# Optimization experiments

Hardware: AMD Instinct MI355X
Metric: run time of the kernel (lower is better)

## Reference

```python
import jax, jax.numpy as jnp
import numpy as np
import heapq

VOCAB = 50257
EMBED = 128
SEED = 0


def _build_padded_paths(vocab_size: int, seed: int):
    """Build a Huffman tree over random word counts and return padded
    per-leaf path index / code / mask arrays: [V, max_depth]."""
    rng = np.random.default_rng(seed)
    counts = rng.integers(1, 1000, size=vocab_size).astype(np.int64)
    # node = (value, left, right); leaves: 0..V-1, internal: V..2V-2
    heap = [(int(counts[i]), i, (i, None, None)) for i in range(vocab_size)]
    heapq.heapify(heap)
    nv = vocab_size
    while len(heap) > 1:
        c1, _, n1 = heapq.heappop(heap)
        c2, _, n2 = heapq.heappop(heap)
        heapq.heappush(heap, (c1 + c2, nv, (nv, n1, n2)))
        nv += 1
    root = heap[0][2]
    assert root[0] == 2 * vocab_size - 2
    path_idx = [None] * vocab_size
    path_code = [None] * vocab_size
    stack = [(root, [], [])]
    while stack:
        (val, left, right), idx, code = stack.pop()
        if left is None:  # leaf
            path_idx[val] = idx
            path_code[val] = code
        else:
            ni = idx + [val - vocab_size]
            stack.append((left, ni, code + [0.0]))
            stack.append((right, ni, code + [1.0]))
    max_d = max(len(p) for p in path_idx)
    I = np.zeros((vocab_size, max_d), dtype=np.int32)
    C = np.zeros((vocab_size, max_d), dtype=np.float32)
    M = np.zeros((vocab_size, max_d), dtype=np.float32)
    for v in range(vocab_size):
        L = len(path_idx[v])
        I[v, :L] = path_idx[v]
        C[v, :L] = path_code[v]
        M[v, :L] = 1.0
    return jnp.asarray(I), jnp.asarray(C), jnp.asarray(M)


def setup_inputs() -> dict:
    key = jax.random.key(0)
    k1, k2, k3 = jax.random.split(key, 3)
    embedding = jax.random.normal(k1, (128, 1, 256, EMBED), dtype=jnp.float32)
    target = jax.random.randint(k2, (128, 1, 256), 0, VOCAB, dtype=jnp.int32)
    fc = jax.random.uniform(k3, (VOCAB - 1, EMBED), dtype=jnp.float32)  # torch.rand init
    path_idx, path_code, path_mask = _build_padded_paths(VOCAB, SEED)
    return {"embedding": embedding, "target": target, "fc": fc,
            "path_idx": path_idx, "path_code": path_code, "path_mask": path_mask}


def reference(embedding, target, fc, path_idx, path_code, path_mask):
    emb = embedding.reshape(-1, embedding.shape[-1])          # [T, H]
    t = target.reshape(-1)                                     # [T]
    idx = path_idx[t]                                          # [T, D]
    code = path_code[t]                                        # [T, D]
    mask = path_mask[t]                                        # [T, D]
    w = fc[idx]                                                # [T, D, H] gathered rows
    logits = jnp.einsum('th,tdh->td', emb, w)                  # [T, D]
    # binary_cross_entropy_with_logits, elementwise, stable
    bce = jnp.maximum(logits, 0.0) - logits * code + jnp.log1p(jnp.exp(-jnp.abs(logits)))
    return jnp.sum(bce * mask) / jnp.sum(mask)
```

## Files before the change

### kernel.cpp

```cpp
#include <hip/hip_runtime.h>

#define TILE    16
#define BLOCK   256
#define EMBED   128
#define VOCAB   50257
#define ESTRIDE 132
#define NPART   2048

__global__ __launch_bounds__(256) void hs_pack(
    const float* __restrict__ fc, ushort* __restrict__ out, int n)
{
    const int stride = gridDim.x * 256 * 8;
    for (int i = (blockIdx.x * 256 + threadIdx.x) * 8; i < n; i += stride) {
        const uint4 a = *(const uint4*)(fc + i);
        const uint4 b = *(const uint4*)(fc + i + 4);
        ushort r[8];
        const uint* u = &a.x;
        #pragma unroll
        for (int j = 0; j < 4; ++j)
            r[j] = (ushort)((u[j] + 0x7FFFu + ((u[j] >> 16) & 1u)) >> 16);
        const uint* v = &b.x;
        #pragma unroll
        for (int j = 0; j < 4; ++j)
            r[4 + j] = (ushort)((v[j] + 0x7FFFu + ((v[j] >> 16) & 1u)) >> 16);
        *(uint4*)(out + i) = *(uint4*)r;
    }
}

__global__ __launch_bounds__(BLOCK) void hs_main_bf16(
    const float* __restrict__ emb,
    const int*   __restrict__ target,
    const ushort* __restrict__ fcb,
    const int*   __restrict__ path_idx,
    const float* __restrict__ path_code,
    const float* __restrict__ path_mask,
    int T, int D,
    float* __restrict__ partial_b,
    float* __restrict__ partial_c)
{
    extern __shared__ char smem[];
    float* se  = (float*)smem;
    int2*  sic = (int2*)(smem + TILE * ESTRIDE * 4);
    __shared__ float sb[BLOCK / 64];
    __shared__ float sc[BLOCK / 64];

    const int tok0 = blockIdx.x * TILE;
    const int ntok = min(TILE, T - tok0);

    const float4* g4 = (const float4*)(emb + (size_t)tok0 * EMBED);
    for (int j = threadIdx.x; j < TILE * (EMBED / 4); j += BLOCK) {
        const int f = j * 4, tk = f >> 7, kk = f & 127;
        float4 v = make_float4(0.f, 0.f, 0.f, 0.f);
        if (tk < ntok) v = g4[j];
        *(float4*)&se[tk * ESTRIDE + kk] = v;
    }
    for (int j = threadIdx.x; j < TILE * D; j += BLOCK) {
        const int tk = j & (TILE - 1), d = j >> 4;
        int2 m = make_int2(0, __float_as_int(-1.0f));
        if (tk < ntok) {
            const int v = target[tok0 + tk];
            const size_t po = (size_t)v * D + d;
            if (path_mask[po] != 0.f)
                m = make_int2(path_idx[po], __float_as_int(path_code[po]));
        }
        sic[j] = m;
    }
    __syncthreads();

    const int wave = threadIdx.x >> 6;
    const int g    = (threadIdx.x >> 2) & 15;
    const int sub  = threadIdx.x & 3;

    float accb = 0.f, accc = 0.f;

    const int items = TILE * D;
    for (int it = wave * 16; it < items; it += 64) {
        const int item = it + g;
        const int2 m = sic[item];
        const float code = __int_as_float(m.y);
        if (code >= 0.f) {
            const char*   wrow = (const char*)(fcb + (size_t)m.x * EMBED);
            const float4* e4   = (const float4*)&se[g * ESTRIDE];
            float s0 = 0.f, s1 = 0.f;
            #pragma unroll
            for (int k = 0; k < 4; ++k) {
                const int c8 = k * 4 + sub;
                const uint4  wv = *(const uint4*)(wrow + (c8 << 4));
                const float4 ea = e4[c8 * 2];
                const float4 eb = e4[c8 * 2 + 1];
                s0 = fmaf(ea.x, __uint_as_float(wv.x << 16),        s0);
                s1 = fmaf(ea.y, __uint_as_float(wv.x & 0xFFFF0000u), s1);
                s0 = fmaf(ea.z, __uint_as_float(wv.y << 16),        s0);
                s1 = fmaf(ea.w, __uint_as_float(wv.y & 0xFFFF0000u), s1);
                s0 = fmaf(eb.x, __uint_as_float(wv.z << 16),        s0);
                s1 = fmaf(eb.y, __uint_as_float(wv.z & 0xFFFF0000u), s1);
                s0 = fmaf(eb.z, __uint_as_float(wv.w << 16),        s0);
                s1 = fmaf(eb.w, __uint_as_float(wv.w & 0xFFFF0000u), s1);
            }
            float x = s0 + s1;
            x += __shfl_xor(x, 1);
            x += __shfl_xor(x, 2);
            accb += fmaxf(x, 0.f) - x * code + __logf(1.f + __expf(-fabsf(x)));
            accc += 1.f;
        }
    }

    #pragma unroll
    for (int o = 32; o > 0; o >>= 1) {
        accb += __shfl_xor(accb, o);
        accc += __shfl_xor(accc, o);
    }
    const int lane = threadIdx.x & 63;
    if (lane == 0) { sb[wave] = accb; sc[wave] = accc; }
    __syncthreads();
    if (threadIdx.x == 0) {
        float b = 0.f, c = 0.f;
        #pragma unroll
        for (int i = 0; i < BLOCK / 64; ++i) { b += sb[i]; c += sc[i]; }
        partial_b[blockIdx.x] = b;
        partial_c[blockIdx.x] = c;
    }
}

__global__ __launch_bounds__(BLOCK) void hs_main_f32(
    const float* __restrict__ emb, const int* __restrict__ target,
    const float* __restrict__ fc,  const int* __restrict__ path_idx,
    const float* __restrict__ path_code, const float* __restrict__ path_mask,
    int T, int D, float* __restrict__ partial_b, float* __restrict__ partial_c)
{
    extern __shared__ char smem[];
    float* se  = (float*)smem;
    int2*  sic = (int2*)(smem + TILE * ESTRIDE * 4);
    __shared__ float sb[BLOCK / 64];
    __shared__ float sc[BLOCK / 64];

    const int tok0 = blockIdx.x * TILE;
    const int ntok = min(TILE, T - tok0);

    const float4* g4 = (const float4*)(emb + (size_t)tok0 * EMBED);
    for (int j = threadIdx.x; j < TILE * (EMBED / 4); j += BLOCK) {
        const int f = j * 4, tk = f >> 7, kk = f & 127;
        float4 v = make_float4(0.f, 0.f, 0.f, 0.f);
        if (tk < ntok) v = g4[j];
        *(float4*)&se[tk * ESTRIDE + kk] = v;
    }
    for (int j = threadIdx.x; j < TILE * D; j += BLOCK) {
        const int tk = j & (TILE - 1), d = j >> 4;
        int2 m = make_int2(0, __float_as_int(-1.0f));
        if (tk < ntok) {
            const int v = target[tok0 + tk];
            const size_t po = (size_t)v * D + d;
            if (path_mask[po] != 0.f)
                m = make_int2(path_idx[po], __float_as_int(path_code[po]));
        }
        sic[j] = m;
    }
    __syncthreads();

    const int wave = threadIdx.x >> 6;
    const int g    = (threadIdx.x >> 2) & 15;
    const int sub  = threadIdx.x & 3;
    float accb = 0.f, accc = 0.f;

    const int items = TILE * D;
    for (int it = wave * 16; it < items; it += 64) {
        const int item = it + g;
        const int2 m = sic[item];
        const float code = __int_as_float(m.y);
        if (code >= 0.f) {
            const float4* w4 = (const float4*)(fc + (size_t)m.x * EMBED);
            const float4* e4 = (const float4*)&se[g * ESTRIDE];
            float s0 = 0.f, s1 = 0.f, s2 = 0.f, s3 = 0.f;
            #pragma unroll
            for (int k = 0; k < 8; ++k) {
                const float4 w  = w4[k * 4 + sub];
                const float4 ev = e4[k * 4 + sub];
                s0 = fmaf(ev.x, w.x, s0); s1 = fmaf(ev.y, w.y, s1);
                s2 = fmaf(ev.z, w.z, s2); s3 = fmaf(ev.w, w.w, s3);
            }
            float x = (s0 + s1) + (s2 + s3);
            x += __shfl_xor(x, 1); x += __shfl_xor(x, 2);
            accb += fmaxf(x, 0.f) - x * code + __logf(1.f + __expf(-fabsf(x)));
            accc += 1.f;
        }
    }
    #pragma unroll
    for (int o = 32; o > 0; o >>= 1) {
        accb += __shfl_xor(accb, o);
        accc += __shfl_xor(accc, o);
    }
    const int lane = threadIdx.x & 63;
    if (lane == 0) { sb[wave] = accb; sc[wave] = accc; }
    __syncthreads();
    if (threadIdx.x == 0) {
        float b = 0.f, c = 0.f;
        #pragma unroll
        for (int i = 0; i < BLOCK / 64; ++i) { b += sb[i]; c += sc[i]; }
        partial_b[blockIdx.x] = b;
        partial_c[blockIdx.x] = c;
    }
}

__global__ __launch_bounds__(256) void hs_finalize(
    const float* __restrict__ pb, const float* __restrict__ pc,
    int n, float* __restrict__ out)
{
    __shared__ double rb[256];
    __shared__ double rc[256];
    double sbv = 0.0, scv = 0.0;
    for (int i = threadIdx.x; i < n; i += 256) {
        sbv += (double)pb[i];
        scv += (double)pc[i];
    }
    rb[threadIdx.x] = sbv; rc[threadIdx.x] = scv;
    __syncthreads();
    for (int s = 128; s > 0; s >>= 1) {
        if (threadIdx.x < s) {
            rb[threadIdx.x] += rb[threadIdx.x + s];
            rc[threadIdx.x] += rc[threadIdx.x + s];
        }
        __syncthreads();
    }
    if (threadIdx.x == 0) out[0] = (float)(rb[0] / rc[0]);
}

extern "C" void kernel_launch(void* const* d_in, const int* in_sizes, int n_in,
                              void* d_out, int out_size, void* d_ws, size_t ws_size,
                              hipStream_t stream) {
    const float* emb   = (const float*)d_in[0];
    const int*   tgt   = (const int*)  d_in[1];
    const float* fc    = (const float*)d_in[2];
    const int*   pidx  = (const int*)  d_in[3];
    const float* pcode = (const float*)d_in[4];
    const float* pmask = (const float*)d_in[5];

    const int T   = in_sizes[1];
    const int D   = in_sizes[3] / VOCAB;
    const int nfc = in_sizes[2];

    const int nblocks = (T + TILE - 1) / TILE;
    const size_t shmem = (size_t)TILE * ESTRIDE * 4 + (size_t)TILE * D * 8;

    float* pb = (float*)d_ws;
    float* pc = pb + NPART;
    ushort* fcb = (ushort*)((char*)d_ws + 2 * NPART * sizeof(float));
    const size_t need = 2 * NPART * sizeof(float) + (size_t)nfc * sizeof(ushort);
    float* out = (float*)d_out;

    if (ws_size >= need) {
        hs_pack<<<1024, 256, 0, stream>>>(fc, fcb, nfc);
        hs_main_bf16<<<nblocks, BLOCK, shmem, stream>>>(
            emb, tgt, fcb, pidx, pcode, pmask, T, D, pb, pc);
    } else {
        hs_main_f32<<<nblocks, BLOCK, shmem, stream>>>(
            emb, tgt, fc, pidx, pcode, pmask, T, D, pb, pc);
    }
    hs_finalize<<<1, 256, 0, stream>>>(pb, pc, nblocks, out);
}
```

Before: 35.50 us.

## Prefetch all path-row gathers up front with fully unrolled templated kernel

```diff
diff --git a/kernel.cpp b/kernel.cpp
--- a/kernel.cpp
+++ b/kernel.cpp
@@ -27,7 +27,8 @@
     }
 }
 
-__global__ __launch_bounds__(BLOCK) void hs_main_bf16(
+template <int NITER>
+__global__ __launch_bounds__(BLOCK) void hs_main_pipe(
     const float* __restrict__ emb,
     const int*   __restrict__ target,
     const ushort* __restrict__ fcb,
@@ -38,6 +39,114 @@
     float* __restrict__ partial_b,
     float* __restrict__ partial_c)
 {
+    constexpr int DP = NITER * 4;
+    extern __shared__ char smem[];
+    float* se  = (float*)smem;
+    int2*  sic = (int2*)(smem + TILE * ESTRIDE * 4);
+    __shared__ float sb[BLOCK / 64];
+    __shared__ float sc[BLOCK / 64];
+
+    const int tok0 = blockIdx.x * TILE;
+    const int ntok = min(TILE, T - tok0);
+
+    const float4* g4 = (const float4*)(emb + (size_t)tok0 * EMBED);
+    for (int j = threadIdx.x; j < TILE * (EMBED / 4); j += BLOCK) {
+        const int f = j * 4, tk = f >> 7, kk = f & 127;
+        float4 v = make_float4(0.f, 0.f, 0.f, 0.f);
+        if (tk < ntok) v = g4[j];
+        *(float4*)&se[tk * ESTRIDE + kk] = v;
+    }
+    for (int j = threadIdx.x; j < TILE * DP; j += BLOCK) {
+        const int tk = j & (TILE - 1), d = j >> 4;
+        int2 m = make_int2(0, __float_as_int(-1.0f));
+        if (tk < ntok && d < D) {
+            const int v = target[tok0 + tk];
+            const size_t po = (size_t)v * D + d;
+            if (path_mask[po] != 0.f)
+                m = make_int2(path_idx[po], __float_as_int(path_code[po]));
+        }
+        sic[j] = m;
+    }
+    __syncthreads();
+
+    const int wave = threadIdx.x >> 6;
+    const int g    = (threadIdx.x >> 2) & 15;
+    const int sub  = threadIdx.x & 3;
+
+    const float4* e4 = (const float4*)&se[g * ESTRIDE];
+    float4 ef[8];
+    #pragma unroll
+    for (int k = 0; k < 4; ++k) {
+        ef[2 * k]     = e4[(k * 4 + sub) * 2];
+        ef[2 * k + 1] = e4[(k * 4 + sub) * 2 + 1];
+    }
+
+    int2 meta[NITER];
+    #pragma unroll
+    for (int i = 0; i < NITER; ++i)
+        meta[i] = sic[wave * 16 + i * 64 + g];
+
+    uint4 wv[NITER][4];
+    #pragma unroll
+    for (int i = 0; i < NITER; ++i) {
+        const ushort* wrow = fcb + (size_t)meta[i].x * EMBED;
+        #pragma unroll
+        for (int k = 0; k < 4; ++k)
+            wv[i][k] = *(const uint4*)(wrow + (size_t)((k * 4 + sub) << 3));
+    }
+
+    float accb = 0.f, accc = 0.f;
+    #pragma unroll
+    for (int i = 0; i < NITER; ++i) {
+        const float code = __int_as_float(meta[i].y);
+        const float wgt  = code >= 0.f ? 1.f : 0.f;
+        const float cd   = fmaxf(code, 0.f);
+        float s0 = 0.f, s1 = 0.f;
+        #pragma unroll
+        for (int k = 0; k < 4; ++k) {
+            const uint4  w  = wv[i][k];
+            const float4 ea = ef[2 * k];
+            const float4 eb = ef[2 * k + 1];
+            s0 = fmaf(ea.x, __uint_as_float(w.x << 16),         s0);
+            s1 = fmaf(ea.y, __uint_as_float(w.x & 0xFFFF0000u), s1);
+            s0 = fmaf(ea.z, __uint_as_float(w.y << 16),         s0);
+            s1 = fmaf(ea.w, __uint_as_float(w.y & 0xFFFF0000u), s1);
+            s0 = fmaf(eb.x, __uint_as_float(w.z << 16),         s0);
+            s1 = fmaf(eb.y, __uint_as_float(w.z & 0xFFFF0000u), s1);
+            s0 = fmaf(eb.z, __uint_as_float(w.w << 16),         s0);
+            s1 = fmaf(eb.w, __uint_as_float(w.w & 0xFFFF0000u), s1);
+        }
+        float x = s0 + s1;
+        x += __shfl_xor(x, 1);
+        x += __shfl_xor(x, 2);
+        accb += wgt * (fmaxf(x, 0.f) - x * cd
+                       + __logf(1.f + __expf(-fabsf(x))));
+        accc += wgt;
+    }
+
+    #pragma unroll
+    for (int o = 32; o > 0; o >>= 1) {
+        accb += __shfl_xor(accb, o);
+        accc += __shfl_xor(accc, o);
+    }
+    const int lane = threadIdx.x & 63;
+    if (lane == 0) { sb[wave] = accb; sc[wave] = accc; }
+    __syncthreads();
+    if (threadIdx.x == 0) {
+        float b = 0.f, c = 0.f;
+        #pragma unroll
+        for (int i = 0; i < BLOCK / 64; ++i) { b += sb[i]; c += sc[i]; }
+        partial_b[blockIdx.x] = b;
+        partial_c[blockIdx.x] = c;
+    }
+}
+
+__global__ __launch_bounds__(BLOCK) void hs_main_bf16(
+    const float* __restrict__ emb, const int* __restrict__ target,
+    const ushort* __restrict__ fcb, const int* __restrict__ path_idx,
+    const float* __restrict__ path_code, const float* __restrict__ path_mask,
+    int T, int D, float* __restrict__ partial_b, float* __restrict__ partial_c)
+{
     extern __shared__ char smem[];
     float* se  = (float*)smem;
     int2*  sic = (int2*)(smem + TILE * ESTRIDE * 4);
@@ -70,32 +179,30 @@
     const int wave = threadIdx.x >> 6;
     const int g    = (threadIdx.x >> 2) & 15;
     const int sub  = threadIdx.x & 3;
-
     float accb = 0.f, accc = 0.f;
 
     const int items = TILE * D;
     for (int it = wave * 16; it < items; it += 64) {
-        const int item = it + g;
-        const int2 m = sic[item];
+        const int2 m = sic[it + g];
         const float code = __int_as_float(m.y);
         if (code >= 0.f) {
-            const char*   wrow = (const char*)(fcb + (size_t)m.x * EMBED);
+            const ushort* wrow = fcb + (size_t)m.x * EMBED;
             const float4* e4   = (const float4*)&se[g * ESTRIDE];
             float s0 = 0.f, s1 = 0.f;
             #pragma unroll
             for (int k = 0; k < 4; ++k) {
                 const int c8 = k * 4 + sub;
-                const uint4  wv = *(const uint4*)(wrow + (c8 << 4));
+                const uint4  w  = *(const uint4*)(wrow + (c8 << 3));
                 const float4 ea = e4[c8 * 2];
                 const float4 eb = e4[c8 * 2 + 1];
-                s0 = fmaf(ea.x, __uint_as_float(wv.x << 16),        s0);
-                s1 = fmaf(ea.y, __uint_as_float(wv.x & 0xFFFF0000u), s1);
-                s0 = fmaf(ea.z, __uint_as_float(wv.y << 16),        s0);
-                s1 = fmaf(ea.w, __uint_as_float(wv.y & 0xFFFF0000u), s1);
-                s0 = fmaf(eb.x, __uint_as_float(wv.z << 16),        s0);
-                s1 = fmaf(eb.y, __uint_as_float(wv.z & 0xFFFF0000u), s1);
-                s0 = fmaf(eb.z, __uint_as_float(wv.w << 16),        s0);
-                s1 = fmaf(eb.w, __uint_as_float(wv.w & 0xFFFF0000u), s1);
+                s0 = fmaf(ea.x, __uint_as_float(w.x << 16),         s0);
+                s1 = fmaf(ea.y, __uint_as_float(w.x & 0xFFFF0000u), s1);
+                s0 = fmaf(ea.z, __uint_as_float(w.y << 16),         s0);
+                s1 = fmaf(ea.w, __uint_as_float(w.y & 0xFFFF0000u), s1);
+                s0 = fmaf(eb.x, __uint_as_float(w.z << 16),         s0);
+                s1 = fmaf(eb.y, __uint_as_float(w.z & 0xFFFF0000u), s1);
+                s0 = fmaf(eb.z, __uint_as_float(w.w << 16),         s0);
+                s1 = fmaf(eb.w, __uint_as_float(w.w & 0xFFFF0000u), s1);
             }
             float x = s0 + s1;
             x += __shfl_xor(x, 1);
@@ -104,7 +211,6 @@
             accc += 1.f;
         }
     }
-
     #pragma unroll
     for (int o = 32; o > 0; o >>= 1) {
         accb += __shfl_xor(accb, o);
@@ -164,8 +270,7 @@
 
     const int items = TILE * D;
     for (int it = wave * 16; it < items; it += 64) {
-        const int item = it + g;
-        const int2 m = sic[item];
+        const int2 m = sic[it + g];
         const float code = __int_as_float(m.y);
         if (code >= 0.f) {
             const float4* w4 = (const float4*)(fc + (size_t)m.x * EMBED);
@@ -239,7 +344,10 @@
     const int nfc = in_sizes[2];
 
     const int nblocks = (T + TILE - 1) / TILE;
-    const size_t shmem = (size_t)TILE * ESTRIDE * 4 + (size_t)TILE * D * 8;
+    const int niter   = (D + 3) / 4;
+    const int DP      = niter * 4;
+    const size_t shmem_pipe = (size_t)TILE * ESTRIDE * 4 + (size_t)TILE * DP * 8;
+    const size_t shmem_loop = (size_t)TILE * ESTRIDE * 4 + (size_t)TILE * D * 8;
 
     float* pb = (float*)d_ws;
     float* pc = pb + NPART;
@@ -249,10 +357,29 @@
 
     if (ws_size >= need) {
         hs_pack<<<1024, 256, 0, stream>>>(fc, fcb, nfc);
-        hs_main_bf16<<<nblocks, BLOCK, shmem, stream>>>(
-            emb, tgt, fcb, pidx, pcode, pmask, T, D, pb, pc);
+        switch (niter) {
+        case 1: hs_main_pipe<1><<<nblocks, BLOCK, shmem_pipe, stream>>>(
+                    emb, tgt, fcb, pidx, pcode, pmask, T, D, pb, pc); break;
+        case 2: hs_main_pipe<2><<<nblocks, BLOCK, shmem_pipe, stream>>>(
+                    emb, tgt, fcb, pidx, pcode, pmask, T, D, pb, pc); break;
+        case 3: hs_main_pipe<3><<<nblocks, BLOCK, shmem_pipe, stream>>>(
+                    emb, tgt, fcb, pidx, pcode, pmask, T, D, pb, pc); break;
+        case 4: hs_main_pipe<4><<<nblocks, BLOCK, shmem_pipe, stream>>>(
+                    emb, tgt, fcb, pidx, pcode, pmask, T, D, pb, pc); break;
+        case 5: hs_main_pipe<5><<<nblocks, BLOCK, shmem_pipe, stream>>>(
+                    emb, tgt, fcb, pidx, pcode, pmask, T, D, pb, pc); break;
+        case 6: hs_main_pipe<6><<<nblocks, BLOCK, shmem_pipe, stream>>>(
+                    emb, tgt, fcb, pidx, pcode, pmask, T, D, pb, pc); break;
+        case 7: hs_main_pipe<7><<<nblocks, BLOCK, shmem_pipe, stream>>>(
+                    emb, tgt, fcb, pidx, pcode, pmask, T, D, pb, pc); break;
+        case 8: hs_main_pipe<8><<<nblocks, BLOCK, shmem_pipe, stream>>>(
+                    emb, tgt, fcb, pidx, pcode, pmask, T, D, pb, pc); break;
+        default:
+            hs_main_bf16<<<nblocks, BLOCK, shmem_loop, stream>>>(
+                emb, tgt, fcb, pidx, pcode, pmask, T, D, pb, pc); break;
+        }
     } else {
-        hs_main_f32<<<nblocks, BLOCK, shmem, stream>>>(
+        hs_main_f32<<<nblocks, BLOCK, shmem_loop, stream>>>(
             emb, tgt, fc, pidx, pcode, pmask, T, D, pb, pc);
     }
     hs_finalize<<<1, 256, 0, stream>>>(pb, pc, nblocks, out);
```

After: 34.20 us. -3.7%, faster.
